# Kernel optimization log

Measured on AMD Instinct MI355X. Metric: run time of the kernel, lower is better.

Reference implementation:

```python
import jax, jax.numpy as jnp
import numpy as np

B, S, D = 2, 2048, 2048
H, DP = 16, 128
WINDOW = 512


def setup_inputs() -> dict:
    key = jax.random.key(0)
    ks = jax.random.split(key, 9)
    sc = 0.02
    return {
        "x": jax.random.normal(ks[0], (B, S, D), dtype=jnp.float32),
        "wq": jax.random.normal(ks[1], (D, H * DP), dtype=jnp.float32) * sc,
        "bq": jax.random.normal(ks[2], (H * DP,), dtype=jnp.float32) * sc,
        "wk": jax.random.normal(ks[3], (D, H * DP), dtype=jnp.float32) * sc,
        "bk": jax.random.normal(ks[4], (H * DP,), dtype=jnp.float32) * sc,
        "wv": jax.random.normal(ks[5], (D, H * DP), dtype=jnp.float32) * sc,
        "bv": jax.random.normal(ks[6], (H * DP,), dtype=jnp.float32) * sc,
        "wo": jax.random.normal(ks[7], (H * DP,), dtype=jnp.float32) * sc,
        "bo": jax.random.normal(ks[8], (1,), dtype=jnp.float32) * sc,
    }


def _sliding_window_mask(seq_len, window):
    q_idx = jnp.arange(seq_len)[:, None]
    kv_idx = jnp.arange(seq_len)[None, :]
    return (q_idx >= kv_idx) & (q_idx - kv_idx < window)


def reference(x, wq, bq, wk, bk, wv, bv, wo, bo):
    b, s, _ = x.shape
    # QKV projections -> (B, H, S, DP)
    q = (x @ wq + bq).reshape(b, s, H, DP).transpose(0, 2, 1, 3)
    k = (x @ wk + bk).reshape(b, s, H, DP).transpose(0, 2, 1, 3)
    v = (x @ wv + bv).reshape(b, s, H, DP).transpose(0, 2, 1, 3)
    scale = 1.0 / np.sqrt(DP).astype(np.float32)
    scores = jnp.einsum("bhqd,bhkd->bhqk", q, k) * scale  # (B,H,S,S)
    mask = _sliding_window_mask(s, WINDOW)
    scores = jnp.where(mask, scores, jnp.finfo(scores.dtype).min)
    attn = jax.nn.softmax(scores, axis=-1)
    o = jnp.einsum("bhqk,bhkd->bhqd", attn, v)  # (B,H,S,DP)
    o = o.transpose(0, 2, 1, 3).reshape(b, s, H * DP)
    return o @ wo + bo[0]  # (B, S)
```

## Files before the change

### kernel.cpp

```cpp
#include <hip/hip_runtime.h>

typedef unsigned short USH;
typedef __bf16 v8bf __attribute__((ext_vector_type(8)));
typedef float v4f __attribute__((ext_vector_type(4)));
typedef unsigned short us8 __attribute__((ext_vector_type(8)));

#define SB 2048
#define DD 2048
#define NH 16
#define DPH 128

__device__ __forceinline__ USH f2bf(float f) {
  unsigned u = __float_as_uint(f);
  u = u + 0x7fffu + ((u >> 16) & 1u);
  return (USH)(u >> 16);
}

#define GL16(gp, lp)                                                   \
  __builtin_amdgcn_global_load_lds(                                    \
      (const __attribute__((address_space(1))) void*)(gp),             \
      (__attribute__((address_space(3))) void*)(lp), 16, 0, 0)

__global__ __launch_bounds__(256) void k_prep(const float* __restrict__ x,
    const float* __restrict__ wq, const float* __restrict__ wk,
    const float* __restrict__ wvf, const float* __restrict__ bvf,
    const float* __restrict__ wo,
    USH* __restrict__ xb, USH* __restrict__ wqt, USH* __restrict__ wkt,
    USH* __restrict__ wvoT, float* __restrict__ bvo) {
  __shared__ USH tl[64][72];
  __shared__ float red[256];
  const int bid = blockIdx.x;
  const int t = threadIdx.x;
  if (bid < 4096) {
    const int i = (bid * 256 + t) * 8;
    const float4 a = *(const float4*)&x[i];
    const float4 b = *(const float4*)&x[i + 4];
    v8bf o;
    o[0] = (__bf16)a.x; o[1] = (__bf16)a.y; o[2] = (__bf16)a.z; o[3] = (__bf16)a.w;
    o[4] = (__bf16)b.x; o[5] = (__bf16)b.y; o[6] = (__bf16)b.z; o[7] = (__bf16)b.w;
    *(v8bf*)&xb[i] = o;
  } else if (bid < 6144) {
    const int rel = bid - 4096;
    const int z = rel >> 10, rem = rel & 1023;
    const float* w = z ? wk : wq;
    USH* wt = z ? wkt : wqt;
    const int k0 = (rem >> 5) * 64, j0 = (rem & 31) * 64;
#pragma unroll
    for (int p = 0; p < 4; ++p) {
      const int r = p * 16 + (t >> 4);
      const int c = (t & 15) * 4;
      const float4 v = *(const float4*)&w[(size_t)(k0 + r) * DD + j0 + c];
      tl[c + 0][r] = f2bf(v.x);
      tl[c + 1][r] = f2bf(v.y);
      tl[c + 2][r] = f2bf(v.z);
      tl[c + 3][r] = f2bf(v.w);
    }
    __syncthreads();
#pragma unroll
    for (int p = 0; p < 2; ++p) {
      const int j = p * 32 + (t >> 3);
      const int seg = (t & 7) * 8;
      us8 v = *(const us8*)&tl[j][seg];
      *(us8*)&wt[(size_t)(j0 + j) * DD + k0 + seg] = v;
    }
  } else {
    const int d = bid - 6144;
    const float* src = (d == DD) ? bvf : (wvf + (size_t)d * DD);
    const float4 a0 = *(const float4*)&src[t * 8];
    const float4 a1 = *(const float4*)&src[t * 8 + 4];
    const float4 w0 = *(const float4*)&wo[t * 8];
    const float4 w1 = *(const float4*)&wo[t * 8 + 4];
    red[t] = a0.x * w0.x + a0.y * w0.y + a0.z * w0.z + a0.w * w0.w +
             a1.x * w1.x + a1.y * w1.y + a1.z * w1.z + a1.w * w1.w;
    __syncthreads();
    for (int s = 8; s > 0; s >>= 1) {
      if ((t & 15) < s) red[t] += red[t + s];
      __syncthreads();
    }
    if ((t & 15) == 0) {
      if (d == DD) bvo[t >> 4] = red[t];
      else wvoT[(size_t)(t >> 4) * DD + d] = f2bf(red[t]);
    }
  }
}

__global__ __launch_bounds__(64) void k_vw2(const USH* __restrict__ xb,
    const USH* __restrict__ wvoT, const float* __restrict__ bvo,
    float* __restrict__ vw) {
  const int lane = threadIdx.x & 63;
  const int lr = lane & 15, g = lane >> 4;
  const int r0 = blockIdx.x * 16;
  v4f acc = (v4f){0.f, 0.f, 0.f, 0.f};
  const USH* ap = xb + (size_t)(r0 + lr) * DD + g * 8;
  const USH* bp = wvoT + (size_t)lr * DD + g * 8;
#pragma unroll 4
  for (int kt = 0; kt < 64; ++kt) {
    v8bf af = *(const v8bf*)(ap + kt * 32);
    v8bf bf = *(const v8bf*)(bp + kt * 32);
    acc = __builtin_amdgcn_mfma_f32_16x16x32_bf16(af, bf, acc, 0, 0, 0);
  }
  const float bb = bvo[lr];
#pragma unroll
  for (int rr = 0; rr < 4; ++rr) {
    const int row = r0 + g * 4 + rr;
    vw[((size_t)(row >> 11) * NH + lr) * SB + (row & 2047)] = acc[rr] + bb;
  }
}

__global__ __launch_bounds__(512, 2) void k_gemm256(
    const USH* __restrict__ xb,
    const USH* __restrict__ wqt, const USH* __restrict__ wkt,
    const float* __restrict__ bq, const float* __restrict__ bk,
    USH* __restrict__ Qb, USH* __restrict__ Kb) {
  __shared__ USH As[2][16384];
  __shared__ USH Bs[2][16384];
  const int fid = blockIdx.x;
  const int nid = (fid & 7) * 32 + (fid >> 3);
  const int z = nid >> 7;
  const int ty = (nid >> 3) & 15, tx = nid & 7;
  const int row0 = ty * 256, col0 = tx * 256;
  const USH* wt = z ? wkt : wqt;
  const float* bias = z ? bk : bq;
  USH* outp = z ? Kb : Qb;
  const float qscale = z ? 1.0f : 0.08838834764831845f;
  const int t = threadIdx.x;
  const int w = t >> 6, lane = t & 63;
  const int lr = lane & 15, g = lane >> 4;
  const int wr = w >> 2, wc = w & 3;
  size_t gA[4], gB[4];
  int ldsOff[4];
#pragma unroll
  for (int q = 0; q < 4; ++q) {
    const int p = q * 512 + t;
    const int row = p >> 3, ps = p & 7;
    const int sl = ps ^ (row & 7);
    gA[q] = (size_t)(row0 + row) * DD + sl * 8;
    gB[q] = (size_t)(col0 + row) * DD + sl * 8;
    ldsOff[q] = p * 8;
  }
  const int swz = (g ^ (lr & 7)) * 8;
  const int k1o = swz ^ 32;
  const int rowA = wr * 128 + lr;
  const int rowB = wc * 64 + lr;

  v4f acc[8][4];
#pragma unroll
  for (int i = 0; i < 8; ++i)
#pragma unroll
    for (int j = 0; j < 4; ++j) acc[i][j] = (v4f){0.f, 0.f, 0.f, 0.f};

#pragma unroll
  for (int q = 0; q < 4; ++q) {
    GL16(xb + gA[q], &As[0][ldsOff[q]]);
    GL16(wt + gB[q], &Bs[0][ldsOff[q]]);
  }
#pragma unroll
  for (int q = 0; q < 4; ++q) {
    GL16(xb + gA[q] + 64, &As[1][ldsOff[q]]);
    GL16(wt + gB[q] + 64, &Bs[1][ldsOff[q]]);
  }
  asm volatile("s_waitcnt vmcnt(8)" ::: "memory");
  __builtin_amdgcn_s_barrier();
  __builtin_amdgcn_sched_barrier(0);

  v8bf bfr0[4], bfr1[4], af0[4], af4[4], af1[4], af5[4];
#pragma unroll
  for (int ni = 0; ni < 4; ++ni)
    bfr0[ni] = *(const v8bf*)&Bs[0][(rowB + ni * 16) * 64 + swz];
#pragma unroll
  for (int mi = 0; mi < 4; ++mi)
    af0[mi] = *(const v8bf*)&As[0][(rowA + mi * 16) * 64 + swz];

  for (int kt = 0; kt < 32; ++kt) {
    const int c = kt & 1;
    const USH* Ab = &As[c][0];
    const USH* Bb = &Bs[c][0];
    __builtin_amdgcn_sched_barrier(0);
#pragma unroll
    for (int mi = 0; mi < 4; ++mi)
      af4[mi] = *(const v8bf*)&Ab[(rowA + (mi + 4) * 16) * 64 + swz];
    asm volatile("s_waitcnt lgkmcnt(4)" ::: "memory");
    __builtin_amdgcn_sched_barrier(0);
    __builtin_amdgcn_s_setprio(1);
#pragma unroll
    for (int mi = 0; mi < 4; ++mi)
#pragma unroll
      for (int ni = 0; ni < 4; ++ni)
        acc[mi][ni] = __builtin_amdgcn_mfma_f32_16x16x32_bf16(af0[mi], bfr0[ni], acc[mi][ni], 0, 0, 0);
    __builtin_amdgcn_s_setprio(0);
    __builtin_amdgcn_s_barrier();
    __builtin_amdgcn_sched_barrier(0);
#pragma unroll
    for (int ni = 0; ni < 4; ++ni)
      bfr1[ni] = *(const v8bf*)&Bb[(rowB + ni * 16) * 64 + k1o];
#pragma unroll
    for (int mi = 0; mi < 4; ++mi)
      af1[mi] = *(const v8bf*)&Ab[(rowA + mi * 16) * 64 + k1o];
    asm volatile("s_waitcnt lgkmcnt(8)" ::: "memory");
    __builtin_amdgcn_sched_barrier(0);
    __builtin_amdgcn_s_setprio(1);
#pragma unroll
    for (int mi = 0; mi < 4; ++mi)
#pragma unroll
      for (int ni = 0; ni < 4; ++ni)
        acc[mi + 4][ni] = __builtin_amdgcn_mfma_f32_16x16x32_bf16(af4[mi], bfr0[ni], acc[mi + 4][ni], 0, 0, 0);
    __builtin_amdgcn_s_setprio(0);
    __builtin_amdgcn_s_barrier();
    __builtin_amdgcn_sched_barrier(0);
#pragma unroll
    for (int mi = 0; mi < 4; ++mi)
      af5[mi] = *(const v8bf*)&Ab[(rowA + (mi + 4) * 16) * 64 + k1o];
    asm volatile("s_waitcnt lgkmcnt(4)" ::: "memory");
    __builtin_amdgcn_sched_barrier(0);
    __builtin_amdgcn_s_setprio(1);
#pragma unroll
    for (int mi = 0; mi < 4; ++mi)
#pragma unroll
      for (int ni = 0; ni < 4; ++ni)
        acc[mi][ni] = __builtin_amdgcn_mfma_f32_16x16x32_bf16(af1[mi], bfr1[ni], acc[mi][ni], 0, 0, 0);
    __builtin_amdgcn_s_setprio(0);
    __builtin_amdgcn_s_barrier();
    asm volatile("s_waitcnt lgkmcnt(0)" ::: "memory");
    __builtin_amdgcn_sched_barrier(0);
    __builtin_amdgcn_s_barrier();
    if (kt < 30) {
      const size_t ko = (size_t)(kt + 2) * 64;
#pragma unroll
      for (int q = 0; q < 4; ++q) {
        GL16(xb + gA[q] + ko, &As[c][ldsOff[q]]);
        GL16(wt + gB[q] + ko, &Bs[c][ldsOff[q]]);
      }
    }
    __builtin_amdgcn_s_setprio(1);
#pragma unroll
    for (int mi = 0; mi < 4; ++mi)
#pragma unroll
      for (int ni = 0; ni < 4; ++ni)
        acc[mi + 4][ni] = __builtin_amdgcn_mfma_f32_16x16x32_bf16(af5[mi], bfr1[ni], acc[mi + 4][ni], 0, 0, 0);
    __builtin_amdgcn_s_setprio(0);
    if (kt < 31) {
      if (kt < 30) {
        asm volatile("s_waitcnt vmcnt(8)" ::: "memory");
      } else {
        asm volatile("s_waitcnt vmcnt(0)" ::: "memory");
      }
      __builtin_amdgcn_s_barrier();
      __builtin_amdgcn_sched_barrier(0);
      const USH* An = &As[c ^ 1][0];
      const USH* Bn = &Bs[c ^ 1][0];
#pragma unroll
      for (int ni = 0; ni < 4; ++ni)
        bfr0[ni] = *(const v8bf*)&Bn[(rowB + ni * 16) * 64 + swz];
#pragma unroll
      for (int mi = 0; mi < 4; ++mi)
        af0[mi] = *(const v8bf*)&An[(rowA + mi * 16) * 64 + swz];
    }
  }

  {
    const int hh = (col0 + wc * 64) >> 7;
    const int dpb = (wc & 1) * 64;
    float bvv[4];
#pragma unroll
    for (int ni = 0; ni < 4; ++ni)
      bvv[ni] = bias[col0 + wc * 64 + ni * 16 + lr];
#pragma unroll
    for (int mi = 0; mi < 8; ++mi) {
#pragma unroll
      for (int rr = 0; rr < 4; ++rr) {
        const int row = row0 + wr * 128 + mi * 16 + g * 4 + rr;
        const int bi = row >> 11, s = row & 2047;
        USH* op = &outp[(((size_t)bi * NH + hh) * SB + s) * DPH + dpb + lr];
        op[0]  = f2bf((acc[mi][0][rr] + bvv[0]) * qscale);
        op[16] = f2bf((acc[mi][1][rr] + bvv[1]) * qscale);
        op[32] = f2bf((acc[mi][2][rr] + bvv[2]) * qscale);
        op[48] = f2bf((acc[mi][3][rr] + bvv[3]) * qscale);
      }
    }
  }
}

__global__ __launch_bounds__(512) void k_attn(const USH* __restrict__ Qb,
    const USH* __restrict__ Kb, const float* __restrict__ vw,
    const float* __restrict__ bo, float* __restrict__ out) {
  __shared__ USH Ks[2][8192];
  const int bh = blockIdx.y;
  const int t = threadIdx.x;
  const int wid = t >> 6, lane = t & 63;
  const int lr = lane & 15, g = lane >> 4;
  const int qblk = blockIdx.x * 128;
  const int qb = qblk + wid * 16;
  const USH* Qp = Qb + (size_t)bh * SB * DPH;
  const USH* Kp = Kb + (size_t)bh * SB * DPH;
  const float* vwp = vw + (size_t)bh * SB;

  v8bf qf[4];
  {
    const USH* qrp = Qp + (size_t)(qb + lr) * DPH + g * 8;
#pragma unroll
    for (int kc = 0; kc < 4; ++kc) qf[kc] = *(const v8bf*)(qrp + kc * 32);
  }
  size_t srcO[2];
  int ldsO[2];
#pragma unroll
  for (int q = 0; q < 2; ++q) {
    const int r = t >> 3, ps = t & 7;
    srcO[q] = (size_t)r * DPH + q * 64 + (size_t)(((ps ^ (r & 7)) * 8));
    ldsO[q] = (q * 512 + t) * 8;
  }

  float ls[4], os[4];
#pragma unroll
  for (int r = 0; r < 4; ++r) { ls[r] = 0.f; os[r] = 0.f; }

  const int kb0 = qblk > 511 ? qblk - 512 : 0;
  const int kbend = qblk + 64;

  GL16(Kp + (size_t)kb0 * DPH + srcO[0], &Ks[0][ldsO[0]]);
  GL16(Kp + (size_t)kb0 * DPH + srcO[1], &Ks[0][ldsO[1]]);
  __syncthreads();

  int buf = 0;
  for (int kb = kb0; kb <= kbend; kb += 64, buf ^= 1) {
    if (kb < kbend) {
      GL16(Kp + (size_t)(kb + 64) * DPH + srcO[0], &Ks[buf ^ 1][ldsO[0]]);
      GL16(Kp + (size_t)(kb + 64) * DPH + srcO[1], &Ks[buf ^ 1][ldsO[1]]);
    }
    const USH* base = &Ks[buf][0];
    v4f acc[4];
    float vv[4];
#pragma unroll
    for (int i = 0; i < 4; ++i) {
      v4f a = (v4f){0.f, 0.f, 0.f, 0.f};
#pragma unroll
      for (int kc = 0; kc < 4; ++kc) {
        const int lrow = (kc >> 1) * 64 + i * 16 + lr;
        v8bf kf = *(const v8bf*)&base[lrow * 64 + ((((kc & 1) * 4 + g) ^ (lr & 7)) * 8)];
        a = __builtin_amdgcn_mfma_f32_16x16x32_bf16(qf[kc], kf, a, 0, 0, 0);
      }
      acc[i] = a;
      vv[i] = vwp[kb + i * 16 + lr];
    }
#pragma unroll
    for (int r = 0; r < 4; ++r) {
      const int q_i = qb + g * 4 + r;
      const int k0i = kb + lr;
      float sc0 = acc[0][r], sc1 = acc[1][r], sc2 = acc[2][r], sc3 = acc[3][r];
      sc0 = (k0i <= q_i && q_i - k0i < 512) ? sc0 : -1e30f;
      sc1 = (k0i + 16 <= q_i && q_i - (k0i + 16) < 512) ? sc1 : -1e30f;
      sc2 = (k0i + 32 <= q_i && q_i - (k0i + 32) < 512) ? sc2 : -1e30f;
      sc3 = (k0i + 48 <= q_i && q_i - (k0i + 48) < 512) ? sc3 : -1e30f;
      const float p0 = __expf(sc0);
      const float p1 = __expf(sc1);
      const float p2 = __expf(sc2);
      const float p3 = __expf(sc3);
      ls[r] += (p0 + p1) + (p2 + p3);
      os[r] += (p0 * vv[0] + p1 * vv[1]) + (p2 * vv[2] + p3 * vv[3]);
    }
    __syncthreads();
  }
#pragma unroll
  for (int r = 0; r < 4; ++r) {
    os[r] += __shfl_xor(os[r], 1); ls[r] += __shfl_xor(ls[r], 1);
    os[r] += __shfl_xor(os[r], 2); ls[r] += __shfl_xor(ls[r], 2);
    os[r] += __shfl_xor(os[r], 4); ls[r] += __shfl_xor(ls[r], 4);
    os[r] += __shfl_xor(os[r], 8); ls[r] += __shfl_xor(ls[r], 8);
  }
  if (lr == 0) {
    const float bo16 = bo[0] * 0.0625f;
#pragma unroll
    for (int r = 0; r < 4; ++r)
      atomicAdd(&out[(size_t)(bh >> 4) * SB + qb + g * 4 + r], os[r] / ls[r] + bo16);
  }
}

extern "C" void kernel_launch(void* const* d_in, const int* in_sizes, int n_in,
                              void* d_out, int out_size, void* d_ws, size_t ws_size,
                              hipStream_t stream) {
  const float* x   = (const float*)d_in[0];
  const float* wq  = (const float*)d_in[1];
  const float* bq  = (const float*)d_in[2];
  const float* wk  = (const float*)d_in[3];
  const float* bk  = (const float*)d_in[4];
  const float* wvf = (const float*)d_in[5];
  const float* bvf = (const float*)d_in[6];
  const float* wo  = (const float*)d_in[7];
  const float* bo  = (const float*)d_in[8];
  float* out = (float*)d_out;
  char* ws = (char*)d_ws;

  USH*   wqt = (USH*)(ws);
  USH*   wkt = (USH*)(ws + 8388608);
  USH*   Qb  = (USH*)(ws + 16777216);
  USH*   Kb  = (USH*)(ws + 33554432);
  float* vw  = (float*)(ws + 50331648);
  USH*   wvoT= (USH*)(ws + 50593792);
  float* bvo = (float*)(ws + 50724864);
  USH*   xbf = (USH*)(ws + 50987264);

  hipMemsetAsync(out, 0, (size_t)out_size * sizeof(float), stream);
  k_prep<<<dim3(8193), dim3(256), 0, stream>>>(x, wq, wk, wvf, bvf, wo,
                                               xbf, wqt, wkt, wvoT, bvo);
  k_vw2<<<dim3(256), dim3(64), 0, stream>>>(xbf, wvoT, bvo, vw);
  k_gemm256<<<dim3(256), dim3(512), 0, stream>>>(xbf, wqt, wkt, bq, bk, Qb, Kb);
  k_attn<<<dim3(16, 32), dim3(512), 0, stream>>>(Qb, Kb, vw, bo, out);
}
```

Before: 124.0 us.

## Fold V-projection GEMV into GEMM as extra wave, fold memset into prep

```diff
diff --git a/kernel.cpp b/kernel.cpp
--- a/kernel.cpp
+++ b/kernel.cpp
@@ -26,7 +26,7 @@
     const float* __restrict__ wvf, const float* __restrict__ bvf,
     const float* __restrict__ wo,
     USH* __restrict__ xb, USH* __restrict__ wqt, USH* __restrict__ wkt,
-    USH* __restrict__ wvoT, float* __restrict__ bvo) {
+    USH* __restrict__ wvoT, float* __restrict__ bvo, float* __restrict__ out) {
   __shared__ USH tl[64][72];
   __shared__ float red[256];
   const int bid = blockIdx.x;
@@ -63,7 +63,7 @@
       us8 v = *(const us8*)&tl[j][seg];
       *(us8*)&wt[(size_t)(j0 + j) * DD + k0 + seg] = v;
     }
-  } else {
+  } else if (bid < 8193) {
     const int d = bid - 6144;
     const float* src = (d == DD) ? bvf : (wvf + (size_t)d * DD);
     const float4 a0 = *(const float4*)&src[t * 8];
@@ -81,39 +81,49 @@
       if (d == DD) bvo[t >> 4] = red[t];
       else wvoT[(size_t)(t >> 4) * DD + d] = f2bf(red[t]);
     }
+  } else {
+#pragma unroll
+    for (int i = 0; i < 16; ++i) out[i * 256 + t] = 0.f;
   }
 }
 
-__global__ __launch_bounds__(64) void k_vw2(const USH* __restrict__ xb,
-    const USH* __restrict__ wvoT, const float* __restrict__ bvo,
-    float* __restrict__ vw) {
-  const int lane = threadIdx.x & 63;
-  const int lr = lane & 15, g = lane >> 4;
-  const int r0 = blockIdx.x * 16;
-  v4f acc = (v4f){0.f, 0.f, 0.f, 0.f};
-  const USH* ap = xb + (size_t)(r0 + lr) * DD + g * 8;
-  const USH* bp = wvoT + (size_t)lr * DD + g * 8;
-#pragma unroll 4
-  for (int kt = 0; kt < 64; ++kt) {
-    v8bf af = *(const v8bf*)(ap + kt * 32);
-    v8bf bf = *(const v8bf*)(bp + kt * 32);
-    acc = __builtin_amdgcn_mfma_f32_16x16x32_bf16(af, bf, acc, 0, 0, 0);
-  }
-  const float bb = bvo[lr];
-#pragma unroll
-  for (int rr = 0; rr < 4; ++rr) {
-    const int row = r0 + g * 4 + rr;
-    vw[((size_t)(row >> 11) * NH + lr) * SB + (row & 2047)] = acc[rr] + bb;
-  }
-}
-
-__global__ __launch_bounds__(512, 2) void k_gemm256(
+__global__ __launch_bounds__(576, 1) void k_gemm256(
     const USH* __restrict__ xb,
     const USH* __restrict__ wqt, const USH* __restrict__ wkt,
     const float* __restrict__ bq, const float* __restrict__ bk,
-    USH* __restrict__ Qb, USH* __restrict__ Kb) {
+    USH* __restrict__ Qb, USH* __restrict__ Kb,
+    const USH* __restrict__ wvoT, const float* __restrict__ bvo,
+    float* __restrict__ vw) {
   __shared__ USH As[2][16384];
   __shared__ USH Bs[2][16384];
+  const int t = threadIdx.x;
+  const int w = t >> 6;
+  if (w == 8) {
+    const int lane2 = t & 63;
+    const int lr2 = lane2 & 15, g2 = lane2 >> 4;
+    const int r0 = blockIdx.x * 16;
+    v4f acc2 = (v4f){0.f, 0.f, 0.f, 0.f};
+    const USH* ap = xb + (size_t)(r0 + lr2) * DD + g2 * 8;
+    const USH* bp = wvoT + (size_t)lr2 * DD + g2 * 8;
+    __builtin_amdgcn_s_barrier();
+    for (int kt = 0; kt < 32; ++kt) {
+      v8bf a0 = *(const v8bf*)(ap + (2 * kt) * 32);
+      v8bf b0 = *(const v8bf*)(bp + (2 * kt) * 32);
+      acc2 = __builtin_amdgcn_mfma_f32_16x16x32_bf16(a0, b0, acc2, 0, 0, 0);
+      v8bf a1 = *(const v8bf*)(ap + (2 * kt + 1) * 32);
+      v8bf b1 = *(const v8bf*)(bp + (2 * kt + 1) * 32);
+      acc2 = __builtin_amdgcn_mfma_f32_16x16x32_bf16(a1, b1, acc2, 0, 0, 0);
+      __builtin_amdgcn_s_barrier();
+      if (kt < 31) __builtin_amdgcn_s_barrier();
+    }
+    const float bb = bvo[lr2];
+#pragma unroll
+    for (int rr = 0; rr < 4; ++rr) {
+      const int row = r0 + g2 * 4 + rr;
+      vw[((size_t)(row >> 11) * NH + lr2) * SB + (row & 2047)] = acc2[rr] + bb;
+    }
+    return;
+  }
   const int fid = blockIdx.x;
   const int nid = (fid & 7) * 32 + (fid >> 3);
   const int z = nid >> 7;
@@ -123,8 +133,7 @@
   const float* bias = z ? bk : bq;
   USH* outp = z ? Kb : Qb;
   const float qscale = z ? 1.0f : 0.08838834764831845f;
-  const int t = threadIdx.x;
-  const int w = t >> 6, lane = t & 63;
+  const int lane = t & 63;
   const int lr = lane & 15, g = lane >> 4;
   const int wr = w >> 2, wc = w & 3;
   size_t gA[4], gB[4];
@@ -188,7 +197,6 @@
       for (int ni = 0; ni < 4; ++ni)
         acc[mi][ni] = __builtin_amdgcn_mfma_f32_16x16x32_bf16(af0[mi], bfr0[ni], acc[mi][ni], 0, 0, 0);
     __builtin_amdgcn_s_setprio(0);
-    __builtin_amdgcn_s_barrier();
     __builtin_amdgcn_sched_barrier(0);
 #pragma unroll
     for (int ni = 0; ni < 4; ++ni)
@@ -205,7 +213,6 @@
       for (int ni = 0; ni < 4; ++ni)
         acc[mi + 4][ni] = __builtin_amdgcn_mfma_f32_16x16x32_bf16(af4[mi], bfr0[ni], acc[mi + 4][ni], 0, 0, 0);
     __builtin_amdgcn_s_setprio(0);
-    __builtin_amdgcn_s_barrier();
     __builtin_amdgcn_sched_barrier(0);
 #pragma unroll
     for (int mi = 0; mi < 4; ++mi)
@@ -219,7 +226,6 @@
       for (int ni = 0; ni < 4; ++ni)
         acc[mi][ni] = __builtin_amdgcn_mfma_f32_16x16x32_bf16(af1[mi], bfr1[ni], acc[mi][ni], 0, 0, 0);
     __builtin_amdgcn_s_setprio(0);
-    __builtin_amdgcn_s_barrier();
     asm volatile("s_waitcnt lgkmcnt(0)" ::: "memory");
     __builtin_amdgcn_sched_barrier(0);
     __builtin_amdgcn_s_barrier();
@@ -398,10 +404,9 @@
   float* bvo = (float*)(ws + 50724864);
   USH*   xbf = (USH*)(ws + 50987264);
 
-  hipMemsetAsync(out, 0, (size_t)out_size * sizeof(float), stream);
-  k_prep<<<dim3(8193), dim3(256), 0, stream>>>(x, wq, wk, wvf, bvf, wo,
-                                               xbf, wqt, wkt, wvoT, bvo);
-  k_vw2<<<dim3(256), dim3(64), 0, stream>>>(xbf, wvoT, bvo, vw);
-  k_gemm256<<<dim3(256), dim3(512), 0, stream>>>(xbf, wqt, wkt, bq, bk, Qb, Kb);
+  k_prep<<<dim3(8194), dim3(256), 0, stream>>>(x, wq, wk, wvf, bvf, wo,
+                                               xbf, wqt, wkt, wvoT, bvo, out);
+  k_gemm256<<<dim3(256), dim3(576), 0, stream>>>(xbf, wqt, wkt, bq, bk, Qb, Kb,
+                                                 wvoT, bvo, vw);
   k_attn<<<dim3(16, 32), dim3(512), 0, stream>>>(Qb, Kb, vw, bo, out);
 }
```

New measurement: 415.4 us. 235% more time.
